# Optimization experiments

Measured on AMD Instinct MI355X. Metric: run time of the kernel, lower is better.

## Reference

```python
import jax, jax.numpy as jnp
import numpy as np

N = 50000
E = 1600000
R = 4
D_IN = 128
D_OUT = 128


def setup_inputs() -> dict:
    key = jax.random.key(0)
    ks = jax.random.split(key, 7)
    x = jax.random.normal(ks[0], (N, D_IN), dtype=jnp.float32)
    vals = jax.random.normal(ks[1], (R, E), dtype=jnp.float32) * (1.0 / 32.0)
    weight = jax.random.normal(ks[2], (D_IN, D_OUT), dtype=jnp.float32) * (1.0 / np.sqrt(D_IN))
    filt = jax.random.uniform(ks[3], (R * N, 1), dtype=jnp.float32, minval=0.9, maxval=1.1)
    bias = jnp.zeros((D_OUT,), dtype=jnp.float32)
    rows = jax.random.randint(ks[4], (R, E), 0, N, dtype=jnp.int32)
    cols = jax.random.randint(ks[5], (R, E), 0, N, dtype=jnp.int32)
    return {"x": x, "vals": vals, "weight": weight, "filt": filt,
            "bias": bias, "rows": rows, "cols": cols}


def _spmm(rows, cols, vals, h, n):
    # sparse [n,n] @ dense [n,d] via gather + segment_sum
    return jax.ops.segment_sum(vals[:, None] * h[cols], rows, num_segments=n)


def reference(x, vals, weight, filt, bias, rows, cols):
    n = x.shape[0]
    h = x @ weight                                    # [N, out]
    # cat(d_list, dim=0) @ h  ->  stack of D_i @ h, i.e. [R, N, out]
    y = jax.vmap(lambda r, c, v: _spmm(r, c, v, h, n))(rows, cols, vals)
    y = filt.reshape(rows.shape[0], n, 1) * y         # elementwise wavelet filter
    # cat(d_list, dim=1) @ y  ->  sum_i D_i @ y_i
    out = jax.vmap(lambda r, c, v, yy: _spmm(r, c, v, yy, n))(rows, cols, vals, y).sum(axis=0)
    return out + bias
```

## Files before the change

### kernel.cpp

```cpp
#include <hip/hip_runtime.h>

#define N_NODES 50000
#define N_EDGES 1600000
#define R_WAV 4
#define D 128
#define NB 391
#define CHUNK 4096
#define NPBLK ((N_EDGES + CHUNK - 1) / CHUNK)
#define MAXB 4800

typedef unsigned int u32;
typedef unsigned short u16;

static __device__ inline u16 f2bf(float f) {
    u32 u = __float_as_uint(f);
    u = (u + 0x7FFFu + ((u >> 16) & 1u)) >> 16;
    return (u16)u;
}
static __device__ inline float bf_lo(u32 u) { return __uint_as_float(u << 16); }
static __device__ inline float bf_hi(u32 u) { return __uint_as_float(u & 0xFFFF0000u); }

__global__ __launch_bounds__(128) void gemm_xw(const float* __restrict__ x,
                                               const float* __restrict__ W,
                                               u16* __restrict__ h) {
    __shared__ float xs[4 * 128];
    const int j = threadIdx.x;
    const int row0 = blockIdx.x * 4;
    for (int t = j; t < 512; t += 128) xs[t] = x[(size_t)row0 * D + t];
    __syncthreads();
    float a0 = 0.f, a1 = 0.f, a2 = 0.f, a3 = 0.f;
#pragma unroll 8
    for (int k = 0; k < 128; ++k) {
        const float w = W[k * D + j];
        a0 += xs[k] * w;
        a1 += xs[128 + k] * w;
        a2 += xs[256 + k] * w;
        a3 += xs[384 + k] * w;
    }
    h[(size_t)(row0 + 0) * D + j] = f2bf(a0);
    h[(size_t)(row0 + 1) * D + j] = f2bf(a1);
    h[(size_t)(row0 + 2) * D + j] = f2bf(a2);
    h[(size_t)(row0 + 3) * D + j] = f2bf(a3);
}

__global__ __launch_bounds__(256) void bucket_hist_all(const int* __restrict__ rows_all,
                                                       int* __restrict__ cnt4) {
    __shared__ int lh[NB];
    const int r = blockIdx.y;
    const int* rows = rows_all + (size_t)r * N_EDGES;
    int* cnt = cnt4 + r * NB;
    const int tid = threadIdx.x;
    for (int i = tid; i < NB; i += 256) lh[i] = 0;
    __syncthreads();
    const int e0 = blockIdx.x * CHUNK;
    const int e1 = min(e0 + CHUNK, N_EDGES);
    for (int i = e0 + tid; i < e1; i += 256) atomicAdd(&lh[rows[i] >> 7], 1);
    __syncthreads();
    for (int i = tid; i < NB; i += 256) {
        const int c = lh[i];
        if (c) atomicAdd(&cnt[i], c);
    }
}

__global__ __launch_bounds__(512) void scan_buckets_all(const int* __restrict__ cnt4,
                                                        int* __restrict__ bptr4,
                                                        int* __restrict__ bcur4) {
    __shared__ int sa[512], sb[512];
    const int r = blockIdx.x;
    const int* cnt = cnt4 + r * NB;
    int* bptr = bptr4 + r * (NB + 1);
    int* bcur = bcur4 + r * NB;
    const int tid = threadIdx.x;
    const int v = (tid < NB) ? cnt[tid] : 0;
    sa[tid] = v;
    int* cur = sa;
    int* nxt = sb;
    for (int d = 1; d < 512; d <<= 1) {
        __syncthreads();
        int t = cur[tid];
        if (tid >= d) t += cur[tid - d];
        nxt[tid] = t;
        int* tmp = cur; cur = nxt; nxt = tmp;
    }
    __syncthreads();
    const int excl = cur[tid] - v;
    if (tid <= NB) bptr[tid] = excl;
    if (tid < NB) bcur[tid] = excl;
}

__global__ __launch_bounds__(256) void partition_kernel(const int* __restrict__ rows,
                                                        const int* __restrict__ cols,
                                                        const float* __restrict__ vals,
                                                        int* __restrict__ bcur,
                                                        int2* __restrict__ cv) {
    __shared__ int lh[NB], lptr[NB], lcur[NB], lbase[NB];
    __shared__ int sa[256], sb[256];
    __shared__ int2 st[CHUNK];
    const int tid = threadIdx.x;
    for (int i = tid; i < NB; i += 256) lh[i] = 0;
    __syncthreads();
    const int e0 = blockIdx.x * CHUNK;
    const int e1 = min(e0 + CHUNK, N_EDGES);
    const int cnt = e1 - e0;
    for (int i = e0 + tid; i < e1; i += 256) atomicAdd(&lh[rows[i] >> 7], 1);
    __syncthreads();
    const int p0 = (2 * tid < NB) ? lh[2 * tid] : 0;
    const int p1 = (2 * tid + 1 < NB) ? lh[2 * tid + 1] : 0;
    sa[tid] = p0 + p1;
    int* cur = sa;
    int* nxt = sb;
    for (int d = 1; d < 256; d <<= 1) {
        __syncthreads();
        int t = cur[tid];
        if (tid >= d) t += cur[tid - d];
        nxt[tid] = t;
        int* tmp = cur; cur = nxt; nxt = tmp;
    }
    __syncthreads();
    const int pe = cur[tid] - (p0 + p1);
    if (2 * tid < NB)     { lptr[2 * tid] = pe;           lcur[2 * tid] = pe; }
    if (2 * tid + 1 < NB) { lptr[2 * tid + 1] = pe + p0;  lcur[2 * tid + 1] = pe + p0; }
    __syncthreads();
    for (int i = e0 + tid; i < e1; i += 256) {
        const int row = rows[i];
        const int b = row >> 7;
        const int pos = atomicAdd(&lcur[b], 1);
        st[pos] = make_int2((int)(((u32)row << 16) | (u32)cols[i]), __float_as_int(vals[i]));
    }
    __syncthreads();
    for (int b = tid; b < NB; b += 256) {
        const int c = lh[b];
        int gb = 0;
        if (c) gb = atomicAdd(&bcur[b], c);
        lbase[b] = gb - lptr[b];
    }
    __syncthreads();
    for (int i = tid; i < cnt; i += 256) {
        const int2 e = st[i];
        const int b = (int)((u32)e.x >> 23);
        cv[lbase[b] + i] = e;
    }
}

__global__ __launch_bounds__(256) void bucket_csr(const int* __restrict__ bptr,
                                                  const int2* __restrict__ cv,
                                                  u32* __restrict__ cv4,
                                                  int* __restrict__ row_ptr) {
    __shared__ int lh[128], lexcl[128], lcur[128];
    __shared__ u32 st[MAXB];
    const int b = blockIdx.x;
    const int s = bptr[b], e1 = bptr[b + 1];
    const int cnt = e1 - s;
    const int tid = threadIdx.x;
    if (tid < 128) lh[tid] = 0;
    __syncthreads();
    for (int i = s + tid; i < e1; i += 256)
        atomicAdd(&lh[((u32)cv[i].x >> 16) & 127u], 1);
    __syncthreads();
    if (tid < 64) {
        const int p0 = lh[2 * tid], p1 = lh[2 * tid + 1];
        int ssum = p0 + p1;
#pragma unroll
        for (int d = 1; d < 64; d <<= 1) {
            const int t = __shfl_up(ssum, d, 64);
            if (tid >= d) ssum += t;
        }
        const int pe = ssum - (p0 + p1);
        lexcl[2 * tid] = pe;          lcur[2 * tid] = pe;
        lexcl[2 * tid + 1] = pe + p0; lcur[2 * tid + 1] = pe + p0;
    }
    __syncthreads();
    for (int i = s + tid; i < e1; i += 256) {
        const int2 E = cv[i];
        const int lr = (int)(((u32)E.x >> 16) & 127u);
        const int pos = atomicAdd(&lcur[lr], 1);
        if (pos < MAXB)
            st[pos] = ((u32)f2bf(__int_as_float(E.y)) << 16) | ((u32)E.x & 0xFFFFu);
    }
    __syncthreads();
    const int wb = (cnt < MAXB) ? cnt : MAXB;
    for (int i = tid; i < wb; i += 256) cv4[s + i] = st[i];
    if (tid < 128) {
        const int row = (b << 7) + tid;
        if (row < N_NODES) row_ptr[row] = s + lexcl[tid];
    }
    if (b == 0 && tid == 0) row_ptr[N_NODES] = N_EDGES;
}

__global__ __launch_bounds__(256) void spmm1(const int* __restrict__ row_ptr,
                                             const u32* __restrict__ cvp,
                                             const u32* __restrict__ h2,
                                             const float* __restrict__ filt_r,
                                             u32* __restrict__ y2) {
    const int row = __builtin_amdgcn_readfirstlane(blockIdx.x * 4 + (threadIdx.x >> 6));
    const int lane = threadIdx.x & 63;
    const int half = lane >> 5;
    const int l = lane & 31;
    int e = row_ptr[row];
    const int end = row_ptr[row + 1];
    float a0 = 0.f, a1 = 0.f, a2 = 0.f, a3 = 0.f;
    float b0 = 0.f, b1 = 0.f, b2 = 0.f, b3 = 0.f;
    for (; e + 8 <= end; e += 8) {
        const u32 c0 = cvp[e], c1 = cvp[e + 1], c2 = cvp[e + 2], c3 = cvp[e + 3];
        const u32 c4 = cvp[e + 4], c5 = cvp[e + 5], c6 = cvp[e + 6], c7 = cvp[e + 7];
        const u32 uA = half ? c1 : c0;
        const u32 uB = half ? c3 : c2;
        const u32 uC = half ? c5 : c4;
        const u32 uD = half ? c7 : c6;
        const uint2 gA = *(const uint2*)(h2 + (uA & 0xFFFFu) * 64 + 2 * l);
        const uint2 gB = *(const uint2*)(h2 + (uB & 0xFFFFu) * 64 + 2 * l);
        const uint2 gC = *(const uint2*)(h2 + (uC & 0xFFFFu) * 64 + 2 * l);
        const uint2 gD = *(const uint2*)(h2 + (uD & 0xFFFFu) * 64 + 2 * l);
        const float vA = __uint_as_float(uA & 0xFFFF0000u);
        const float vB = __uint_as_float(uB & 0xFFFF0000u);
        const float vC = __uint_as_float(uC & 0xFFFF0000u);
        const float vD = __uint_as_float(uD & 0xFFFF0000u);
        a0 += vA * bf_lo(gA.x); a1 += vA * bf_hi(gA.x);
        a2 += vA * bf_lo(gA.y); a3 += vA * bf_hi(gA.y);
        b0 += vB * bf_lo(gB.x); b1 += vB * bf_hi(gB.x);
        b2 += vB * bf_lo(gB.y); b3 += vB * bf_hi(gB.y);
        a0 += vC * bf_lo(gC.x); a1 += vC * bf_hi(gC.x);
        a2 += vC * bf_lo(gC.y); a3 += vC * bf_hi(gC.y);
        b0 += vD * bf_lo(gD.x); b1 += vD * bf_hi(gD.x);
        b2 += vD * bf_lo(gD.y); b3 += vD * bf_hi(gD.y);
    }
    for (; e < end; e += 2) {
        const u32 c0 = cvp[e];
        const u32 c1 = (e + 1 < end) ? cvp[e + 1] : 0u;
        const u32 uA = half ? c1 : c0;
        const uint2 gA = *(const uint2*)(h2 + (uA & 0xFFFFu) * 64 + 2 * l);
        const float vA = __uint_as_float(uA & 0xFFFF0000u);
        a0 += vA * bf_lo(gA.x); a1 += vA * bf_hi(gA.x);
        a2 += vA * bf_lo(gA.y); a3 += vA * bf_hi(gA.y);
    }
    a0 += b0; a1 += b1; a2 += b2; a3 += b3;
    a0 += __shfl_xor(a0, 32, 64);
    a1 += __shfl_xor(a1, 32, 64);
    a2 += __shfl_xor(a2, 32, 64);
    a3 += __shfl_xor(a3, 32, 64);
    const float f = filt_r[row];
    if (half == 0) {
        uint2 o;
        o.x = (u32)f2bf(f * a0) | ((u32)f2bf(f * a1) << 16);
        o.y = (u32)f2bf(f * a2) | ((u32)f2bf(f * a3) << 16);
        *(uint2*)(y2 + (size_t)row * 64 + 2 * l) = o;
    }
}

template <bool FIRST>
__global__ __launch_bounds__(256) void spmm2(const int* __restrict__ row_ptr,
                                             const u32* __restrict__ cvp,
                                             const u32* __restrict__ y2,
                                             const float* __restrict__ bias,
                                             float* __restrict__ out) {
    const int row = __builtin_amdgcn_readfirstlane(blockIdx.x * 4 + (threadIdx.x >> 6));
    const int lane = threadIdx.x & 63;
    const int half = lane >> 5;
    const int l = lane & 31;
    int e = row_ptr[row];
    const int end = row_ptr[row + 1];
    float a0 = 0.f, a1 = 0.f, a2 = 0.f, a3 = 0.f;
    float b0 = 0.f, b1 = 0.f, b2 = 0.f, b3 = 0.f;
    for (; e + 8 <= end; e += 8) {
        const u32 c0 = cvp[e], c1 = cvp[e + 1], c2 = cvp[e + 2], c3 = cvp[e + 3];
        const u32 c4 = cvp[e + 4], c5 = cvp[e + 5], c6 = cvp[e + 6], c7 = cvp[e + 7];
        const u32 uA = half ? c1 : c0;
        const u32 uB = half ? c3 : c2;
        const u32 uC = half ? c5 : c4;
        const u32 uD = half ? c7 : c6;
        const uint2 gA = *(const uint2*)(y2 + (uA & 0xFFFFu) * 64 + 2 * l);
        const uint2 gB = *(const uint2*)(y2 + (uB & 0xFFFFu) * 64 + 2 * l);
        const uint2 gC = *(const uint2*)(y2 + (uC & 0xFFFFu) * 64 + 2 * l);
        const uint2 gD = *(const uint2*)(y2 + (uD & 0xFFFFu) * 64 + 2 * l);
        const float vA = __uint_as_float(uA & 0xFFFF0000u);
        const float vB = __uint_as_float(uB & 0xFFFF0000u);
        const float vC = __uint_as_float(uC & 0xFFFF0000u);
        const float vD = __uint_as_float(uD & 0xFFFF0000u);
        a0 += vA * bf_lo(gA.x); a1 += vA * bf_hi(gA.x);
        a2 += vA * bf_lo(gA.y); a3 += vA * bf_hi(gA.y);
        b0 += vB * bf_lo(gB.x); b1 += vB * bf_hi(gB.x);
        b2 += vB * bf_lo(gB.y); b3 += vB * bf_hi(gB.y);
        a0 += vC * bf_lo(gC.x); a1 += vC * bf_hi(gC.x);
        a2 += vC * bf_lo(gC.y); a3 += vC * bf_hi(gC.y);
        b0 += vD * bf_lo(gD.x); b1 += vD * bf_hi(gD.x);
        b2 += vD * bf_lo(gD.y); b3 += vD * bf_hi(gD.y);
    }
    for (; e < end; e += 2) {
        const u32 c0 = cvp[e];
        const u32 c1 = (e + 1 < end) ? cvp[e + 1] : 0u;
        const u32 uA = half ? c1 : c0;
        const uint2 gA = *(const uint2*)(y2 + (uA & 0xFFFFu) * 64 + 2 * l);
        const float vA = __uint_as_float(uA & 0xFFFF0000u);
        a0 += vA * bf_lo(gA.x); a1 += vA * bf_hi(gA.x);
        a2 += vA * bf_lo(gA.y); a3 += vA * bf_hi(gA.y);
    }
    a0 += b0; a1 += b1; a2 += b2; a3 += b3;
    a0 += __shfl_xor(a0, 32, 64);
    a1 += __shfl_xor(a1, 32, 64);
    a2 += __shfl_xor(a2, 32, 64);
    a3 += __shfl_xor(a3, 32, 64);
    if (half == 0) {
        float* op = out + (size_t)row * D + 4 * l;
        if (FIRST) {
            const float4 bb = *(const float4*)(bias + 4 * l);
            *(float4*)op = make_float4(a0 + bb.x, a1 + bb.y, a2 + bb.z, a3 + bb.w);
        } else {
            const float4 cc = *(const float4*)op;
            *(float4*)op = make_float4(cc.x + a0, cc.y + a1, cc.z + a2, cc.w + a3);
        }
    }
}

extern "C" void kernel_launch(void* const* d_in, const int* in_sizes, int n_in,
                              void* d_out, int out_size, void* d_ws, size_t ws_size,
                              hipStream_t stream) {
    const float* x    = (const float*)d_in[0];
    const float* vals = (const float*)d_in[1];
    const float* W    = (const float*)d_in[2];
    const float* filt = (const float*)d_in[3];
    const float* bias = (const float*)d_in[4];
    const int*   rows = (const int*)d_in[5];
    const int*   cols = (const int*)d_in[6];
    float* out = (float*)d_out;

    char* ws = (char*)d_ws;
    u16*  h       = (u16*)(ws);
    u32*  y2      = (u32*)(ws + 12800000);
    int2* cv8     = (int2*)(ws + 25600000);
    u32*  cv4     = (u32*)(ws + 38400000);
    int*  row_ptr = (int*)(ws + 44800512);
    int*  cnt4    = (int*)(ws + 45000576);
    int*  bptr4   = (int*)(ws + 45006976);
    int*  bcur4   = (int*)(ws + 45013376);

    gemm_xw<<<N_NODES / 4, 128, 0, stream>>>(x, W, h);

    hipMemsetAsync(cnt4, 0, 4 * NB * sizeof(int), stream);
    bucket_hist_all<<<dim3(NPBLK, R_WAV), 256, 0, stream>>>(rows, cnt4);
    scan_buckets_all<<<R_WAV, 512, 0, stream>>>(cnt4, bptr4, bcur4);

    for (int r = 0; r < R_WAV; ++r) {
        const int*   rows_r = rows + (size_t)r * N_EDGES;
        const int*   cols_r = cols + (size_t)r * N_EDGES;
        const float* vals_r = vals + (size_t)r * N_EDGES;
        const float* filt_r = filt + (size_t)r * N_NODES;

        partition_kernel<<<NPBLK, 256, 0, stream>>>(rows_r, cols_r, vals_r,
                                                    bcur4 + r * NB, cv8);
        bucket_csr<<<NB, 256, 0, stream>>>(bptr4 + r * (NB + 1), cv8, cv4, row_ptr);
        spmm1<<<N_NODES / 4, 256, 0, stream>>>(row_ptr, cv4, (const u32*)h, filt_r, y2);
        if (r == 0)
            spmm2<true><<<N_NODES / 4, 256, 0, stream>>>(row_ptr, cv4, y2, bias, out);
        else
            spmm2<false><<<N_NODES / 4, 256, 0, stream>>>(row_ptr, cv4, y2, bias, out);
    }
}
```

Before: 737.2 us.

## Slice feature matrices into 32-column planes and pad CSR rows to multiples of eight

The h and y feature matrices are stored as four column-slice planes of 32 bf16 values each. Each SpMM block handles one slice for four rows, with 8 lanes per edge and 8 edges per wave in flight. Row segments are padded with zero entries to a multiple of 8 so the tail loop can run without per-edge bounds checks, and row_ptr is replaced by per-row start/end pairs. The intent is smaller gather footprints per pass, which should improve L2 locality, plus more edges in flight. The cost is four times as many blocks, extra padding traffic, and index entries read once per slice.

Measured after the change: 932.8 us. 26.5% more time.

```diff
diff --git a/kernel.cpp b/kernel.cpp
--- a/kernel.cpp
+++ b/kernel.cpp
@@ -8,6 +8,8 @@
 #define CHUNK 4096
 #define NPBLK ((N_EDGES + CHUNK - 1) / CHUNK)
 #define MAXB 4800
+#define STCAP 5824
+#define BSLACK 1024
 
 typedef unsigned int u32;
 typedef unsigned short u16;
@@ -37,10 +39,11 @@
         a2 += xs[256 + k] * w;
         a3 += xs[384 + k] * w;
     }
-    h[(size_t)(row0 + 0) * D + j] = f2bf(a0);
-    h[(size_t)(row0 + 1) * D + j] = f2bf(a1);
-    h[(size_t)(row0 + 2) * D + j] = f2bf(a2);
-    h[(size_t)(row0 + 3) * D + j] = f2bf(a3);
+    const size_t sb = ((size_t)(j >> 5) * N_NODES) * 32 + (j & 31);
+    h[sb + (size_t)(row0 + 0) * 32] = f2bf(a0);
+    h[sb + (size_t)(row0 + 1) * 32] = f2bf(a1);
+    h[sb + (size_t)(row0 + 2) * 32] = f2bf(a2);
+    h[sb + (size_t)(row0 + 3) * 32] = f2bf(a3);
 }
 
 __global__ __launch_bounds__(256) void bucket_hist_all(const int* __restrict__ rows_all,
@@ -145,12 +148,12 @@
 __global__ __launch_bounds__(256) void bucket_csr(const int* __restrict__ bptr,
                                                   const int2* __restrict__ cv,
                                                   u32* __restrict__ cv4,
-                                                  int* __restrict__ row_ptr) {
-    __shared__ int lh[128], lexcl[128], lcur[128];
-    __shared__ u32 st[MAXB];
+                                                  int2* __restrict__ row_se) {
+    __shared__ int lh[128], lpexcl[128], lcur[128];
+    __shared__ u32 st[STCAP];
+    __shared__ int s_psize;
     const int b = blockIdx.x;
     const int s = bptr[b], e1 = bptr[b + 1];
-    const int cnt = e1 - s;
     const int tid = threadIdx.x;
     if (tid < 128) lh[tid] = 0;
     __syncthreads();
@@ -158,7 +161,8 @@
         atomicAdd(&lh[((u32)cv[i].x >> 16) & 127u], 1);
     __syncthreads();
     if (tid < 64) {
-        const int p0 = lh[2 * tid], p1 = lh[2 * tid + 1];
+        const int c0 = lh[2 * tid], c1 = lh[2 * tid + 1];
+        const int p0 = (c0 + 7) & ~7, p1 = (c1 + 7) & ~7;
         int ssum = p0 + p1;
 #pragma unroll
         for (int d = 1; d < 64; d <<= 1) {
@@ -166,143 +170,144 @@
             if (tid >= d) ssum += t;
         }
         const int pe = ssum - (p0 + p1);
-        lexcl[2 * tid] = pe;          lcur[2 * tid] = pe;
-        lexcl[2 * tid + 1] = pe + p0; lcur[2 * tid + 1] = pe + p0;
-    }
+        lpexcl[2 * tid] = pe;          lcur[2 * tid] = pe;
+        lpexcl[2 * tid + 1] = pe + p0; lcur[2 * tid + 1] = pe + p0;
+        if (tid == 63) s_psize = ssum;
+    }
+    __syncthreads();
+    const int psize = s_psize;
+    for (int i = tid; i < psize; i += 256) st[i] = 0u;
     __syncthreads();
     for (int i = s + tid; i < e1; i += 256) {
         const int2 E = cv[i];
         const int lr = (int)(((u32)E.x >> 16) & 127u);
         const int pos = atomicAdd(&lcur[lr], 1);
-        if (pos < MAXB)
+        if (pos < STCAP)
             st[pos] = ((u32)f2bf(__int_as_float(E.y)) << 16) | ((u32)E.x & 0xFFFFu);
     }
     __syncthreads();
-    const int wb = (cnt < MAXB) ? cnt : MAXB;
-    for (int i = tid; i < wb; i += 256) cv4[s + i] = st[i];
+    const int pbase = s + b * BSLACK;
+    for (int i = tid; i < psize; i += 256) cv4[pbase + i] = st[i];
     if (tid < 128) {
         const int row = (b << 7) + tid;
-        if (row < N_NODES) row_ptr[row] = s + lexcl[tid];
-    }
-    if (b == 0 && tid == 0) row_ptr[N_NODES] = N_EDGES;
-}
-
-__global__ __launch_bounds__(256) void spmm1(const int* __restrict__ row_ptr,
+        if (row < N_NODES) {
+            const int start = pbase + lpexcl[tid];
+            const int pc = (lh[tid] + 7) & ~7;
+            row_se[row] = make_int2(start, start + pc);
+        }
+    }
+}
+
+__global__ __launch_bounds__(256) void spmm1(const int2* __restrict__ row_se,
                                              const u32* __restrict__ cvp,
-                                             const u32* __restrict__ h2,
+                                             const u32* __restrict__ hsl,
                                              const float* __restrict__ filt_r,
-                                             u32* __restrict__ y2) {
-    const int row = __builtin_amdgcn_readfirstlane(blockIdx.x * 4 + (threadIdx.x >> 6));
+                                             u32* __restrict__ ysl) {
+    const int slice = blockIdx.x & 3;
+    const int w = threadIdx.x >> 6;
     const int lane = threadIdx.x & 63;
-    const int half = lane >> 5;
-    const int l = lane & 31;
-    int e = row_ptr[row];
-    const int end = row_ptr[row + 1];
+    const int row = __builtin_amdgcn_readfirstlane((blockIdx.x >> 2) * 4 + w);
+    const int es = lane >> 3;
+    const int cp = lane & 7;
+    const u32* hs = hsl + (size_t)slice * N_NODES * 16;
+    const int2 se = row_se[row];
+    int e = se.x;
+    const int end = se.y;
     float a0 = 0.f, a1 = 0.f, a2 = 0.f, a3 = 0.f;
     float b0 = 0.f, b1 = 0.f, b2 = 0.f, b3 = 0.f;
-    for (; e + 8 <= end; e += 8) {
-        const u32 c0 = cvp[e], c1 = cvp[e + 1], c2 = cvp[e + 2], c3 = cvp[e + 3];
-        const u32 c4 = cvp[e + 4], c5 = cvp[e + 5], c6 = cvp[e + 6], c7 = cvp[e + 7];
-        const u32 uA = half ? c1 : c0;
-        const u32 uB = half ? c3 : c2;
-        const u32 uC = half ? c5 : c4;
-        const u32 uD = half ? c7 : c6;
-        const uint2 gA = *(const uint2*)(h2 + (uA & 0xFFFFu) * 64 + 2 * l);
-        const uint2 gB = *(const uint2*)(h2 + (uB & 0xFFFFu) * 64 + 2 * l);
-        const uint2 gC = *(const uint2*)(h2 + (uC & 0xFFFFu) * 64 + 2 * l);
-        const uint2 gD = *(const uint2*)(h2 + (uD & 0xFFFFu) * 64 + 2 * l);
-        const float vA = __uint_as_float(uA & 0xFFFF0000u);
-        const float vB = __uint_as_float(uB & 0xFFFF0000u);
-        const float vC = __uint_as_float(uC & 0xFFFF0000u);
-        const float vD = __uint_as_float(uD & 0xFFFF0000u);
+    for (; e + 16 <= end; e += 16) {
+        const uint2 c = *(const uint2*)(cvp + e + 2 * es);
+        const uint2 gA = *(const uint2*)(hs + (c.x & 0xFFFFu) * 16 + 2 * cp);
+        const uint2 gB = *(const uint2*)(hs + (c.y & 0xFFFFu) * 16 + 2 * cp);
+        const float vA = __uint_as_float(c.x & 0xFFFF0000u);
+        const float vB = __uint_as_float(c.y & 0xFFFF0000u);
         a0 += vA * bf_lo(gA.x); a1 += vA * bf_hi(gA.x);
         a2 += vA * bf_lo(gA.y); a3 += vA * bf_hi(gA.y);
         b0 += vB * bf_lo(gB.x); b1 += vB * bf_hi(gB.x);
         b2 += vB * bf_lo(gB.y); b3 += vB * bf_hi(gB.y);
-        a0 += vC * bf_lo(gC.x); a1 += vC * bf_hi(gC.x);
-        a2 += vC * bf_lo(gC.y); a3 += vC * bf_hi(gC.y);
-        b0 += vD * bf_lo(gD.x); b1 += vD * bf_hi(gD.x);
-        b2 += vD * bf_lo(gD.y); b3 += vD * bf_hi(gD.y);
-    }
-    for (; e < end; e += 2) {
-        const u32 c0 = cvp[e];
-        const u32 c1 = (e + 1 < end) ? cvp[e + 1] : 0u;
-        const u32 uA = half ? c1 : c0;
-        const uint2 gA = *(const uint2*)(h2 + (uA & 0xFFFFu) * 64 + 2 * l);
-        const float vA = __uint_as_float(uA & 0xFFFF0000u);
-        a0 += vA * bf_lo(gA.x); a1 += vA * bf_hi(gA.x);
-        a2 += vA * bf_lo(gA.y); a3 += vA * bf_hi(gA.y);
-    }
-    a0 += b0; a1 += b1; a2 += b2; a3 += b3;
-    a0 += __shfl_xor(a0, 32, 64);
-    a1 += __shfl_xor(a1, 32, 64);
-    a2 += __shfl_xor(a2, 32, 64);
-    a3 += __shfl_xor(a3, 32, 64);
-    const float f = filt_r[row];
-    if (half == 0) {
-        uint2 o;
-        o.x = (u32)f2bf(f * a0) | ((u32)f2bf(f * a1) << 16);
-        o.y = (u32)f2bf(f * a2) | ((u32)f2bf(f * a3) << 16);
-        *(uint2*)(y2 + (size_t)row * 64 + 2 * l) = o;
-    }
-}
-
-template <bool FIRST>
-__global__ __launch_bounds__(256) void spmm2(const int* __restrict__ row_ptr,
-                                             const u32* __restrict__ cvp,
-                                             const u32* __restrict__ y2,
-                                             const float* __restrict__ bias,
-                                             float* __restrict__ out) {
-    const int row = __builtin_amdgcn_readfirstlane(blockIdx.x * 4 + (threadIdx.x >> 6));
-    const int lane = threadIdx.x & 63;
-    const int half = lane >> 5;
-    const int l = lane & 31;
-    int e = row_ptr[row];
-    const int end = row_ptr[row + 1];
-    float a0 = 0.f, a1 = 0.f, a2 = 0.f, a3 = 0.f;
-    float b0 = 0.f, b1 = 0.f, b2 = 0.f, b3 = 0.f;
-    for (; e + 8 <= end; e += 8) {
-        const u32 c0 = cvp[e], c1 = cvp[e + 1], c2 = cvp[e + 2], c3 = cvp[e + 3];
-        const u32 c4 = cvp[e + 4], c5 = cvp[e + 5], c6 = cvp[e + 6], c7 = cvp[e + 7];
-        const u32 uA = half ? c1 : c0;
-        const u32 uB = half ? c3 : c2;
-        const u32 uC = half ? c5 : c4;
-        const u32 uD = half ? c7 : c6;
-        const uint2 gA = *(const uint2*)(y2 + (uA & 0xFFFFu) * 64 + 2 * l);
-        const uint2 gB = *(const uint2*)(y2 + (uB & 0xFFFFu) * 64 + 2 * l);
-        const uint2 gC = *(const uint2*)(y2 + (uC & 0xFFFFu) * 64 + 2 * l);
-        const uint2 gD = *(const uint2*)(y2 + (uD & 0xFFFFu) * 64 + 2 * l);
-        const float vA = __uint_as_float(uA & 0xFFFF0000u);
-        const float vB = __uint_as_float(uB & 0xFFFF0000u);
-        const float vC = __uint_as_float(uC & 0xFFFF0000u);
-        const float vD = __uint_as_float(uD & 0xFFFF0000u);
+    }
+    if (e < end) {
+        const uint2 c = *(const uint2*)(cvp + e + 2 * es);
+        const u32 ux = (es < 4) ? c.x : 0u;
+        const u32 uy = (es < 4) ? c.y : 0u;
+        const uint2 gA = *(const uint2*)(hs + (ux & 0xFFFFu) * 16 + 2 * cp);
+        const uint2 gB = *(const uint2*)(hs + (uy & 0xFFFFu) * 16 + 2 * cp);
+        const float vA = __uint_as_float(ux & 0xFFFF0000u);
+        const float vB = __uint_as_float(uy & 0xFFFF0000u);
         a0 += vA * bf_lo(gA.x); a1 += vA * bf_hi(gA.x);
         a2 += vA * bf_lo(gA.y); a3 += vA * bf_hi(gA.y);
         b0 += vB * bf_lo(gB.x); b1 += vB * bf_hi(gB.x);
         b2 += vB * bf_lo(gB.y); b3 += vB * bf_hi(gB.y);
-        a0 += vC * bf_lo(gC.x); a1 += vC * bf_hi(gC.x);
-        a2 += vC * bf_lo(gC.y); a3 += vC * bf_hi(gC.y);
-        b0 += vD * bf_lo(gD.x); b1 += vD * bf_hi(gD.x);
-        b2 += vD * bf_lo(gD.y); b3 += vD * bf_hi(gD.y);
-    }
-    for (; e < end; e += 2) {
-        const u32 c0 = cvp[e];
-        const u32 c1 = (e + 1 < end) ? cvp[e + 1] : 0u;
-        const u32 uA = half ? c1 : c0;
-        const uint2 gA = *(const uint2*)(y2 + (uA & 0xFFFFu) * 64 + 2 * l);
-        const float vA = __uint_as_float(uA & 0xFFFF0000u);
+    }
+    a0 += b0; a1 += b1; a2 += b2; a3 += b3;
+    a0 += __shfl_xor(a0, 8, 64);  a1 += __shfl_xor(a1, 8, 64);
+    a2 += __shfl_xor(a2, 8, 64);  a3 += __shfl_xor(a3, 8, 64);
+    a0 += __shfl_xor(a0, 16, 64); a1 += __shfl_xor(a1, 16, 64);
+    a2 += __shfl_xor(a2, 16, 64); a3 += __shfl_xor(a3, 16, 64);
+    a0 += __shfl_xor(a0, 32, 64); a1 += __shfl_xor(a1, 32, 64);
+    a2 += __shfl_xor(a2, 32, 64); a3 += __shfl_xor(a3, 32, 64);
+    const float f = filt_r[row];
+    if (lane < 8) {
+        uint2 o;
+        o.x = (u32)f2bf(f * a0) | ((u32)f2bf(f * a1) << 16);
+        o.y = (u32)f2bf(f * a2) | ((u32)f2bf(f * a3) << 16);
+        *(uint2*)(ysl + (size_t)slice * N_NODES * 16 + (size_t)row * 16 + 2 * lane) = o;
+    }
+}
+
+template <bool FIRST>
+__global__ __launch_bounds__(256) void spmm2(const int2* __restrict__ row_se,
+                                             const u32* __restrict__ cvp,
+                                             const u32* __restrict__ ysl,
+                                             const float* __restrict__ bias,
+                                             float* __restrict__ out) {
+    const int slice = blockIdx.x & 3;
+    const int w = threadIdx.x >> 6;
+    const int lane = threadIdx.x & 63;
+    const int row = __builtin_amdgcn_readfirstlane((blockIdx.x >> 2) * 4 + w);
+    const int es = lane >> 3;
+    const int cp = lane & 7;
+    const u32* ys = ysl + (size_t)slice * N_NODES * 16;
+    const int2 se = row_se[row];
+    int e = se.x;
+    const int end = se.y;
+    float a0 = 0.f, a1 = 0.f, a2 = 0.f, a3 = 0.f;
+    float b0 = 0.f, b1 = 0.f, b2 = 0.f, b3 = 0.f;
+    for (; e + 16 <= end; e += 16) {
+        const uint2 c = *(const uint2*)(cvp + e + 2 * es);
+        const uint2 gA = *(const uint2*)(ys + (c.x & 0xFFFFu) * 16 + 2 * cp);
+        const uint2 gB = *(const uint2*)(ys + (c.y & 0xFFFFu) * 16 + 2 * cp);
+        const float vA = __uint_as_float(c.x & 0xFFFF0000u);
+        const float vB = __uint_as_float(c.y & 0xFFFF0000u);
         a0 += vA * bf_lo(gA.x); a1 += vA * bf_hi(gA.x);
         a2 += vA * bf_lo(gA.y); a3 += vA * bf_hi(gA.y);
+        b0 += vB * bf_lo(gB.x); b1 += vB * bf_hi(gB.x);
+        b2 += vB * bf_lo(gB.y); b3 += vB * bf_hi(gB.y);
+    }
+    if (e < end) {
+        const uint2 c = *(const uint2*)(cvp + e + 2 * es);
+        const u32 ux = (es < 4) ? c.x : 0u;
+        const u32 uy = (es < 4) ? c.y : 0u;
+        const uint2 gA = *(const uint2*)(ys + (ux & 0xFFFFu) * 16 + 2 * cp);
+        const uint2 gB = *(const uint2*)(ys + (uy & 0xFFFFu) * 16 + 2 * cp);
+        const float vA = __uint_as_float(ux & 0xFFFF0000u);
+        const float vB = __uint_as_float(uy & 0xFFFF0000u);
+        a0 += vA * bf_lo(gA.x); a1 += vA * bf_hi(gA.x);
+        a2 += vA * bf_lo(gA.y); a3 += vA * bf_hi(gA.y);
+        b0 += vB * bf_lo(gB.x); b1 += vB * bf_hi(gB.x);
+        b2 += vB * bf_lo(gB.y); b3 += vB * bf_hi(gB.y);
     }
     a0 += b0; a1 += b1; a2 += b2; a3 += b3;
-    a0 += __shfl_xor(a0, 32, 64);
-    a1 += __shfl_xor(a1, 32, 64);
-    a2 += __shfl_xor(a2, 32, 64);
-    a3 += __shfl_xor(a3, 32, 64);
-    if (half == 0) {
-        float* op = out + (size_t)row * D + 4 * l;
+    a0 += __shfl_xor(a0, 8, 64);  a1 += __shfl_xor(a1, 8, 64);
+    a2 += __shfl_xor(a2, 8, 64);  a3 += __shfl_xor(a3, 8, 64);
+    a0 += __shfl_xor(a0, 16, 64); a1 += __shfl_xor(a1, 16, 64);
+    a2 += __shfl_xor(a2, 16, 64); a3 += __shfl_xor(a3, 16, 64);
+    a0 += __shfl_xor(a0, 32, 64); a1 += __shfl_xor(a1, 32, 64);
+    a2 += __shfl_xor(a2, 32, 64); a3 += __shfl_xor(a3, 32, 64);
+    if (lane < 8) {
+        float* op = out + (size_t)row * D + slice * 32 + 4 * lane;
         if (FIRST) {
-            const float4 bb = *(const float4*)(bias + 4 * l);
+            const float4 bb = *(const float4*)(bias + slice * 32 + 4 * lane);
             *(float4*)op = make_float4(a0 + bb.x, a1 + bb.y, a2 + bb.z, a3 + bb.w);
         } else {
             const float4 cc = *(const float4*)op;
@@ -328,10 +333,10 @@
     u32*  y2      = (u32*)(ws + 12800000);
     int2* cv8     = (int2*)(ws + 25600000);
     u32*  cv4     = (u32*)(ws + 38400000);
-    int*  row_ptr = (int*)(ws + 44800512);
-    int*  cnt4    = (int*)(ws + 45000576);
-    int*  bptr4   = (int*)(ws + 45006976);
-    int*  bcur4   = (int*)(ws + 45013376);
+    int2* row_se  = (int2*)(ws + 46800000);
+    int*  cnt4    = (int*)(ws + 47200000);
+    int*  bptr4   = (int*)(ws + 47208192);
+    int*  bcur4   = (int*)(ws + 47216384);
 
     gemm_xw<<<N_NODES / 4, 128, 0, stream>>>(x, W, h);
 
@@ -347,11 +352,11 @@
 
         partition_kernel<<<NPBLK, 256, 0, stream>>>(rows_r, cols_r, vals_r,
                                                     bcur4 + r * NB, cv8);
-        bucket_csr<<<NB, 256, 0, stream>>>(bptr4 + r * (NB + 1), cv8, cv4, row_ptr);
-        spmm1<<<N_NODES / 4, 256, 0, stream>>>(row_ptr, cv4, (const u32*)h, filt_r, y2);
+        bucket_csr<<<NB, 256, 0, stream>>>(bptr4 + r * (NB + 1), cv8, cv4, row_se);
+        spmm1<<<N_NODES, 256, 0, stream>>>(row_se, cv4, (const u32*)h, filt_r, y2);
         if (r == 0)
-            spmm2<true><<<N_NODES / 4, 256, 0, stream>>>(row_ptr, cv4, y2, bias, out);
+            spmm2<true><<<N_NODES, 256, 0, stream>>>(row_se, cv4, y2, bias, out);
         else
-            spmm2<false><<<N_NODES / 4, 256, 0, stream>>>(row_ptr, cv4, y2, bias, out);
-    }
-}
+            spmm2<false><<<N_NODES, 256, 0, stream>>>(row_se, cv4, y2, bias, out);
+    }
+}
```

## Process wavelets in pairs with batched partition/CSR and fused second SpMM

Applied to the files above, without the earlier changes.

Partition and bucket-CSR kernels now handle two wavelets per launch via blockIdx.y, which doubles grid size and cuts the launch count. The second SpMM accumulates two wavelets per row in one kernel, so `out` is read and written half as often. The workspace is re-laid out so y2 aliases the int2 staging buffer, which is dead by the time spmm1 writes y2. The cost is larger per-pair workspace and more cache pressure from two sets of edge arrays.

New measurement: 793.9 us. +7.7%, slower.

```diff
diff --git a/kernel.cpp b/kernel.cpp
--- a/kernel.cpp
+++ b/kernel.cpp
@@ -8,6 +8,7 @@
 #define CHUNK 4096
 #define NPBLK ((N_EDGES + CHUNK - 1) / CHUNK)
 #define MAXB 4800
+#define RP_STRIDE 50016
 
 typedef unsigned int u32;
 typedef unsigned short u16;
@@ -88,14 +89,22 @@
     if (tid < NB) bcur[tid] = excl;
 }
 
-__global__ __launch_bounds__(256) void partition_kernel(const int* __restrict__ rows,
-                                                        const int* __restrict__ cols,
-                                                        const float* __restrict__ vals,
-                                                        int* __restrict__ bcur,
-                                                        int2* __restrict__ cv) {
+__global__ __launch_bounds__(256) void partition_all(const int* __restrict__ rows_all,
+                                                     const int* __restrict__ cols_all,
+                                                     const float* __restrict__ vals_all,
+                                                     int rbase,
+                                                     int* __restrict__ bcur4,
+                                                     int2* __restrict__ cv8base) {
     __shared__ int lh[NB], lptr[NB], lcur[NB], lbase[NB];
     __shared__ int sa[256], sb[256];
     __shared__ int2 st[CHUNK];
+    const int slot = blockIdx.y;
+    const int r = rbase + slot;
+    const int* rows = rows_all + (size_t)r * N_EDGES;
+    const int* cols = cols_all + (size_t)r * N_EDGES;
+    const float* vals = vals_all + (size_t)r * N_EDGES;
+    int* bcur = bcur4 + r * NB;
+    int2* cv = cv8base + (size_t)slot * N_EDGES;
     const int tid = threadIdx.x;
     for (int i = tid; i < NB; i += 256) lh[i] = 0;
     __syncthreads();
@@ -142,12 +151,19 @@
     }
 }
 
-__global__ __launch_bounds__(256) void bucket_csr(const int* __restrict__ bptr,
-                                                  const int2* __restrict__ cv,
-                                                  u32* __restrict__ cv4,
-                                                  int* __restrict__ row_ptr) {
+__global__ __launch_bounds__(256) void bucket_csr_all(const int* __restrict__ bptr4,
+                                                      int rbase,
+                                                      const int2* __restrict__ cv8base,
+                                                      u32* __restrict__ cv4base,
+                                                      int* __restrict__ rp_base) {
     __shared__ int lh[128], lexcl[128], lcur[128];
     __shared__ u32 st[MAXB];
+    const int slot = blockIdx.y;
+    const int r = rbase + slot;
+    const int* bptr = bptr4 + r * (NB + 1);
+    const int2* cv = cv8base + (size_t)slot * N_EDGES;
+    u32* cv4 = cv4base + (size_t)slot * N_EDGES;
+    int* row_ptr = rp_base + slot * RP_STRIDE;
     const int b = blockIdx.x;
     const int s = bptr[b], e1 = bptr[b + 1];
     const int cnt = e1 - s;
@@ -187,19 +203,14 @@
     if (b == 0 && tid == 0) row_ptr[N_NODES] = N_EDGES;
 }
 
-__global__ __launch_bounds__(256) void spmm1(const int* __restrict__ row_ptr,
-                                             const u32* __restrict__ cvp,
-                                             const u32* __restrict__ h2,
-                                             const float* __restrict__ filt_r,
-                                             u32* __restrict__ y2) {
-    const int row = __builtin_amdgcn_readfirstlane(blockIdx.x * 4 + (threadIdx.x >> 6));
-    const int lane = threadIdx.x & 63;
-    const int half = lane >> 5;
-    const int l = lane & 31;
-    int e = row_ptr[row];
-    const int end = row_ptr[row + 1];
-    float a0 = 0.f, a1 = 0.f, a2 = 0.f, a3 = 0.f;
-    float b0 = 0.f, b1 = 0.f, b2 = 0.f, b3 = 0.f;
+static __device__ inline void spmm_accum(const int* __restrict__ rp,
+                                         const u32* __restrict__ cvp,
+                                         const u32* __restrict__ src,
+                                         int row, int half, int l,
+                                         float& a0, float& a1, float& a2, float& a3,
+                                         float& b0, float& b1, float& b2, float& b3) {
+    int e = rp[row];
+    const int end = rp[row + 1];
     for (; e + 8 <= end; e += 8) {
         const u32 c0 = cvp[e], c1 = cvp[e + 1], c2 = cvp[e + 2], c3 = cvp[e + 3];
         const u32 c4 = cvp[e + 4], c5 = cvp[e + 5], c6 = cvp[e + 6], c7 = cvp[e + 7];
@@ -207,10 +218,10 @@
         const u32 uB = half ? c3 : c2;
         const u32 uC = half ? c5 : c4;
         const u32 uD = half ? c7 : c6;
-        const uint2 gA = *(const uint2*)(h2 + (uA & 0xFFFFu) * 64 + 2 * l);
-        const uint2 gB = *(const uint2*)(h2 + (uB & 0xFFFFu) * 64 + 2 * l);
-        const uint2 gC = *(const uint2*)(h2 + (uC & 0xFFFFu) * 64 + 2 * l);
-        const uint2 gD = *(const uint2*)(h2 + (uD & 0xFFFFu) * 64 + 2 * l);
+        const uint2 gA = *(const uint2*)(src + (uA & 0xFFFFu) * 64 + 2 * l);
+        const uint2 gB = *(const uint2*)(src + (uB & 0xFFFFu) * 64 + 2 * l);
+        const uint2 gC = *(const uint2*)(src + (uC & 0xFFFFu) * 64 + 2 * l);
+        const uint2 gD = *(const uint2*)(src + (uD & 0xFFFFu) * 64 + 2 * l);
         const float vA = __uint_as_float(uA & 0xFFFF0000u);
         const float vB = __uint_as_float(uB & 0xFFFF0000u);
         const float vC = __uint_as_float(uC & 0xFFFF0000u);
@@ -228,11 +239,25 @@
         const u32 c0 = cvp[e];
         const u32 c1 = (e + 1 < end) ? cvp[e + 1] : 0u;
         const u32 uA = half ? c1 : c0;
-        const uint2 gA = *(const uint2*)(h2 + (uA & 0xFFFFu) * 64 + 2 * l);
+        const uint2 gA = *(const uint2*)(src + (uA & 0xFFFFu) * 64 + 2 * l);
         const float vA = __uint_as_float(uA & 0xFFFF0000u);
         a0 += vA * bf_lo(gA.x); a1 += vA * bf_hi(gA.x);
         a2 += vA * bf_lo(gA.y); a3 += vA * bf_hi(gA.y);
     }
+}
+
+__global__ __launch_bounds__(256) void spmm1(const int* __restrict__ row_ptr,
+                                             const u32* __restrict__ cvp,
+                                             const u32* __restrict__ h2,
+                                             const float* __restrict__ filt_r,
+                                             u32* __restrict__ y2) {
+    const int row = __builtin_amdgcn_readfirstlane(blockIdx.x * 4 + (threadIdx.x >> 6));
+    const int lane = threadIdx.x & 63;
+    const int half = lane >> 5;
+    const int l = lane & 31;
+    float a0 = 0.f, a1 = 0.f, a2 = 0.f, a3 = 0.f;
+    float b0 = 0.f, b1 = 0.f, b2 = 0.f, b3 = 0.f;
+    spmm_accum(row_ptr, cvp, h2, row, half, l, a0, a1, a2, a3, b0, b1, b2, b3);
     a0 += b0; a1 += b1; a2 += b2; a3 += b3;
     a0 += __shfl_xor(a0, 32, 64);
     a1 += __shfl_xor(a1, 32, 64);
@@ -248,52 +273,22 @@
 }
 
 template <bool FIRST>
-__global__ __launch_bounds__(256) void spmm2(const int* __restrict__ row_ptr,
-                                             const u32* __restrict__ cvp,
-                                             const u32* __restrict__ y2,
-                                             const float* __restrict__ bias,
-                                             float* __restrict__ out) {
+__global__ __launch_bounds__(256) void spmm2_pair(const int* __restrict__ rpa,
+                                                  const int* __restrict__ rpb,
+                                                  const u32* __restrict__ cva,
+                                                  const u32* __restrict__ cvb,
+                                                  const u32* __restrict__ ya,
+                                                  const u32* __restrict__ yb,
+                                                  const float* __restrict__ bias,
+                                                  float* __restrict__ out) {
     const int row = __builtin_amdgcn_readfirstlane(blockIdx.x * 4 + (threadIdx.x >> 6));
     const int lane = threadIdx.x & 63;
     const int half = lane >> 5;
     const int l = lane & 31;
-    int e = row_ptr[row];
-    const int end = row_ptr[row + 1];
     float a0 = 0.f, a1 = 0.f, a2 = 0.f, a3 = 0.f;
     float b0 = 0.f, b1 = 0.f, b2 = 0.f, b3 = 0.f;
-    for (; e + 8 <= end; e += 8) {
-        const u32 c0 = cvp[e], c1 = cvp[e + 1], c2 = cvp[e + 2], c3 = cvp[e + 3];
-        const u32 c4 = cvp[e + 4], c5 = cvp[e + 5], c6 = cvp[e + 6], c7 = cvp[e + 7];
-        const u32 uA = half ? c1 : c0;
-        const u32 uB = half ? c3 : c2;
-        const u32 uC = half ? c5 : c4;
-        const u32 uD = half ? c7 : c6;
-        const uint2 gA = *(const uint2*)(y2 + (uA & 0xFFFFu) * 64 + 2 * l);
-        const uint2 gB = *(const uint2*)(y2 + (uB & 0xFFFFu) * 64 + 2 * l);
-        const uint2 gC = *(const uint2*)(y2 + (uC & 0xFFFFu) * 64 + 2 * l);
-        const uint2 gD = *(const uint2*)(y2 + (uD & 0xFFFFu) * 64 + 2 * l);
-        const float vA = __uint_as_float(uA & 0xFFFF0000u);
-        const float vB = __uint_as_float(uB & 0xFFFF0000u);
-        const float vC = __uint_as_float(uC & 0xFFFF0000u);
-        const float vD = __uint_as_float(uD & 0xFFFF0000u);
-        a0 += vA * bf_lo(gA.x); a1 += vA * bf_hi(gA.x);
-        a2 += vA * bf_lo(gA.y); a3 += vA * bf_hi(gA.y);
-        b0 += vB * bf_lo(gB.x); b1 += vB * bf_hi(gB.x);
-        b2 += vB * bf_lo(gB.y); b3 += vB * bf_hi(gB.y);
-        a0 += vC * bf_lo(gC.x); a1 += vC * bf_hi(gC.x);
-        a2 += vC * bf_lo(gC.y); a3 += vC * bf_hi(gC.y);
-        b0 += vD * bf_lo(gD.x); b1 += vD * bf_hi(gD.x);
-        b2 += vD * bf_lo(gD.y); b3 += vD * bf_hi(gD.y);
-    }
-    for (; e < end; e += 2) {
-        const u32 c0 = cvp[e];
-        const u32 c1 = (e + 1 < end) ? cvp[e + 1] : 0u;
-        const u32 uA = half ? c1 : c0;
-        const uint2 gA = *(const uint2*)(y2 + (uA & 0xFFFFu) * 64 + 2 * l);
-        const float vA = __uint_as_float(uA & 0xFFFF0000u);
-        a0 += vA * bf_lo(gA.x); a1 += vA * bf_hi(gA.x);
-        a2 += vA * bf_lo(gA.y); a3 += vA * bf_hi(gA.y);
-    }
+    spmm_accum(rpa, cva, ya, row, half, l, a0, a1, a2, a3, b0, b1, b2, b3);
+    spmm_accum(rpb, cvb, yb, row, half, l, a0, a1, a2, a3, b0, b1, b2, b3);
     a0 += b0; a1 += b1; a2 += b2; a3 += b3;
     a0 += __shfl_xor(a0, 32, 64);
     a1 += __shfl_xor(a1, 32, 64);
@@ -325,13 +320,13 @@
 
     char* ws = (char*)d_ws;
     u16*  h       = (u16*)(ws);
-    u32*  y2      = (u32*)(ws + 12800000);
-    int2* cv8     = (int2*)(ws + 25600000);
-    u32*  cv4     = (u32*)(ws + 38400000);
-    int*  row_ptr = (int*)(ws + 44800512);
-    int*  cnt4    = (int*)(ws + 45000576);
-    int*  bptr4   = (int*)(ws + 45006976);
-    int*  bcur4   = (int*)(ws + 45013376);
+    u32*  cv4     = (u32*)(ws + 12800000);
+    int*  row_ptr = (int*)(ws + 25600000);
+    int*  cnt4    = (int*)(ws + 26000128);
+    int*  bptr4   = (int*)(ws + 26006384);
+    int*  bcur4   = (int*)(ws + 26012656);
+    int2* cv8     = (int2*)(ws + 26018912);
+    u32*  y2      = (u32*)(ws + 26018912);
 
     gemm_xw<<<N_NODES / 4, 128, 0, stream>>>(x, W, h);
 
@@ -339,19 +334,25 @@
     bucket_hist_all<<<dim3(NPBLK, R_WAV), 256, 0, stream>>>(rows, cnt4);
     scan_buckets_all<<<R_WAV, 512, 0, stream>>>(cnt4, bptr4, bcur4);
 
-    for (int r = 0; r < R_WAV; ++r) {
-        const int*   rows_r = rows + (size_t)r * N_EDGES;
-        const int*   cols_r = cols + (size_t)r * N_EDGES;
-        const float* vals_r = vals + (size_t)r * N_EDGES;
-        const float* filt_r = filt + (size_t)r * N_NODES;
-
-        partition_kernel<<<NPBLK, 256, 0, stream>>>(rows_r, cols_r, vals_r,
-                                                    bcur4 + r * NB, cv8);
-        bucket_csr<<<NB, 256, 0, stream>>>(bptr4 + r * (NB + 1), cv8, cv4, row_ptr);
-        spmm1<<<N_NODES / 4, 256, 0, stream>>>(row_ptr, cv4, (const u32*)h, filt_r, y2);
-        if (r == 0)
-            spmm2<true><<<N_NODES / 4, 256, 0, stream>>>(row_ptr, cv4, y2, bias, out);
+    for (int p = 0; p < 2; ++p) {
+        const int rbase = 2 * p;
+        partition_all<<<dim3(NPBLK, 2), 256, 0, stream>>>(rows, cols, vals, rbase,
+                                                          bcur4, cv8);
+        bucket_csr_all<<<dim3(NB, 2), 256, 0, stream>>>(bptr4, rbase, cv8, cv4, row_ptr);
+        spmm1<<<N_NODES / 4, 256, 0, stream>>>(row_ptr, cv4, (const u32*)h,
+                                               filt + (size_t)rbase * N_NODES,
+                                               y2);
+        spmm1<<<N_NODES / 4, 256, 0, stream>>>(row_ptr + RP_STRIDE, cv4 + N_EDGES,
+                                               (const u32*)h,
+                                               filt + (size_t)(rbase + 1) * N_NODES,
+                                               y2 + 3200000);
+        if (p == 0)
+            spmm2_pair<true><<<N_NODES / 4, 256, 0, stream>>>(
+                row_ptr, row_ptr + RP_STRIDE, cv4, cv4 + N_EDGES,
+                y2, y2 + 3200000, bias, out);
         else
-            spmm2<false><<<N_NODES / 4, 256, 0, stream>>>(row_ptr, cv4, y2, bias, out);
-    }
-}
+            spmm2_pair<false><<<N_NODES / 4, 256, 0, stream>>>(
+                row_ptr, row_ptr + RP_STRIDE, cv4, cv4 + N_EDGES,
+                y2, y2 + 3200000, bias, out);
+    }
+}
```
